# Optimization experiments

Measured on AMD Instinct MI355X. Metric: run time of the kernel, lower is better.

## Reference

```python
import jax, jax.numpy as jnp
import numpy as np

N_IDX = 3_276_800   # total indices shared across all bags
N_BAGS = 16_384     # number of bags (offsets length)
NUM_EMB = 2_000_000 # vocabulary rows per table
DIM = 3             # embedding dim fixed by the module


def setup_inputs() -> dict:
    key = jax.random.key(0)
    k1, k2, k3, k4, k5 = jax.random.split(key, 5)
    eb_input = jax.random.randint(k1, (N_IDX,), 0, NUM_EMB, dtype=jnp.int32)
    eb_offset = jnp.sort(jax.random.randint(k2, (N_BAGS,), 0, N_IDX, dtype=jnp.int32))
    eb_offset = eb_offset.at[0].set(0)  # EmbeddingBag requires offsets[0] == 0
    W0 = jax.random.normal(k3, (NUM_EMB, DIM), dtype=jnp.float32)
    W1 = jax.random.normal(k4, (NUM_EMB, DIM), dtype=jnp.float32)
    W2 = jax.random.normal(k5, (NUM_EMB, DIM), dtype=jnp.float32)
    return {"eb_input": eb_input, "eb_offset": eb_offset, "W0": W0, "W1": W1, "W2": W2}


def _embedding_bag_sum(W, idx, seg_ids, num_bags):
    # gather rows then segment-sum within each bag -> [num_bags, DIM]
    return jax.ops.segment_sum(W[idx], seg_ids, num_segments=num_bags)


def reference(eb_input, eb_offset, W0, W1, W2):
    num_bags = eb_offset.shape[0]
    # bag id of each index position, from the offsets (shared by all 21 bags)
    seg_ids = jnp.searchsorted(eb_offset, jnp.arange(eb_input.shape[0], dtype=eb_offset.dtype), side="right") - 1
    rows = []
    # each group reuses ONE table k times ([module]*k aliases the same module),
    # so cat(k copies of [B,3]).sum(0) == k * per_bag.sum(0)
    for W, mult in ((W0, 5.0), (W1, 10.0), (W2, 6.0)):
        per_bag = _embedding_bag_sum(W, eb_input, seg_ids, num_bags)  # [B, 3]
        rows.append(mult * per_bag.sum(axis=0))                      # [3]
    return jnp.stack(rows)  # [3, 3]
```

## Files before the change

kernel.cpp:

```cpp
#include <hip/hip_runtime.h>


constexpr int BLOCK = 256;
constexpr int WAVES = BLOCK / 64;

constexpr int CBITS = 14;
constexpr int CROWS = 1 << CBITS;
constexpr int MAXKC = 128;
constexpr int GP    = 512;
constexpr int CAPC  = 112;
constexpr int HB    = 1024;
constexpr int SUMG  = 1920;


__global__ __launch_bounds__(BLOCK) void partition_kernel(
    const int* __restrict__ idx,
    unsigned short* __restrict__ region,
    int* __restrict__ counts_T,
    int n, int K)
{
    __shared__ __align__(16) unsigned short buf[MAXKC][CAPC];
    __shared__ int rcnt[MAXKC];

    for (int b = threadIdx.x; b < K; b += BLOCK) rcnt[b] = 0;
    __syncthreads();

    const int g = blockIdx.x;
    const int4* idx4 = (const int4*)idx;
    const int n4 = n >> 2;
    const int per = (n4 + GP - 1) / GP;
    const int start = g * per;
    const int end = min(start + per, n4);

    int4 v[8];
    int cnt = 0;
    for (int i = start + threadIdx.x; i < end; i += BLOCK)
        v[cnt++] = idx4[i];

    for (int j = 0; j < cnt; ++j) {
        int4 w = v[j];
        int xs[4] = {w.x, w.y, w.z, w.w};
#pragma unroll
        for (int h = 0; h < 4; ++h) {
            int b = xs[h] >> CBITS, lo = xs[h] & (CROWS - 1);
            int pos = atomicAdd(&rcnt[b], 1);
            if (pos < CAPC) buf[b][pos] = (unsigned short)lo;
        }
    }
    if (g == 0 && threadIdx.x == 0) {
        for (int i = n4 << 2; i < n; ++i) {
            int x = idx[i];
            int b = x >> CBITS, lo = x & (CROWS - 1);
            int pos = atomicAdd(&rcnt[b], 1);
            if (pos < CAPC) buf[b][pos] = (unsigned short)lo;
        }
    }
    __syncthreads();

    for (int b = threadIdx.x; b < K; b += BLOCK) {
        int c = rcnt[b]; if (c > CAPC) c = CAPC;
        unsigned short* cell = region + ((size_t)b * GP + g) * CAPC;
        const int ng = (c + 7) >> 3;
        for (int j = 0; j < ng; ++j)
            *(uint4*)(cell + j * 8) = *(const uint4*)&buf[b][j * 8];
        counts_T[b * GP + g] = c;
    }
}


__global__ __launch_bounds__(HB) void hist_build_kernel(
    const unsigned short* __restrict__ region,
    const int* __restrict__ counts_T,
    int* __restrict__ counts)
{
    __shared__ unsigned int histp[CROWS / 2];
    __shared__ int scnt[GP];
    const int b = blockIdx.x;

    for (int j = threadIdx.x; j < CROWS / 2; j += HB) histp[j] = 0u;
    for (int g = threadIdx.x; g < GP; g += HB) scnt[g] = counts_T[b * GP + g];
    __syncthreads();

    constexpr int GPC = CAPC / 8;
    constexpr int NG  = GP * GPC;
    const uint4* reg4 = (const uint4*)(region + (size_t)b * GP * CAPC);
    for (int j = threadIdx.x; j < NG; j += HB) {
        int g = j / GPC;
        int q = j - g * GPC;
        uint4 v = reg4[j];
        int valid = scnt[g] - q * 8;
        if (valid >= 8) {
            atomicAdd(&histp[(v.x & 0xFFFFu) >> 1], 1u << (((v.x) & 1u) << 4));
            atomicAdd(&histp[(v.x >> 16) >> 1],     1u << (((v.x >> 16) & 1u) << 4));
            atomicAdd(&histp[(v.y & 0xFFFFu) >> 1], 1u << (((v.y) & 1u) << 4));
            atomicAdd(&histp[(v.y >> 16) >> 1],     1u << (((v.y >> 16) & 1u) << 4));
            atomicAdd(&histp[(v.z & 0xFFFFu) >> 1], 1u << (((v.z) & 1u) << 4));
            atomicAdd(&histp[(v.z >> 16) >> 1],     1u << (((v.z >> 16) & 1u) << 4));
            atomicAdd(&histp[(v.w & 0xFFFFu) >> 1], 1u << (((v.w) & 1u) << 4));
            atomicAdd(&histp[(v.w >> 16) >> 1],     1u << (((v.w >> 16) & 1u) << 4));
        } else if (valid > 0) {
            unsigned vv[4] = {v.x, v.y, v.z, v.w};
#pragma unroll
            for (int h = 0; h < 4; ++h) {
                unsigned lo0 = vv[h] & 0xFFFFu, lo1 = vv[h] >> 16;
                if (valid > 2 * h)     atomicAdd(&histp[lo0 >> 1], 1u << ((lo0 & 1u) << 4));
                if (valid > 2 * h + 1) atomicAdd(&histp[lo1 >> 1], 1u << ((lo1 & 1u) << 4));
            }
        }
    }
    __syncthreads();

    int4* out4 = (int4*)(counts + ((size_t)b << CBITS));
    for (int j = threadIdx.x; j < CROWS / 4; j += HB) {
        unsigned u0 = histp[2 * j], u1 = histp[2 * j + 1];
        int4 val;
        val.x = (int)(u0 & 0xFFFFu);
        val.y = (int)(u0 >> 16);
        val.z = (int)(u1 & 0xFFFFu);
        val.w = (int)(u1 >> 16);
        out4[j] = val;
    }
}


__global__ __launch_bounds__(BLOCK) void weighted_sum_v4(
    const int* __restrict__ counts,
    const float* __restrict__ W0,
    const float* __restrict__ W1,
    const float* __restrict__ W2,
    float* __restrict__ partials,
    int nrows)
{
    float s[9];
#pragma unroll
    for (int k = 0; k < 9; ++k) s[k] = 0.0f;
    const int tid = blockIdx.x * BLOCK + threadIdx.x;
    const int stride = gridDim.x * BLOCK;
    const int nt = nrows >> 2;
    const int4*   c4  = (const int4*)counts;
    const float4* W04 = (const float4*)W0;
    const float4* W14 = (const float4*)W1;
    const float4* W24 = (const float4*)W2;
    for (int t = tid; t < nt; t += stride) {
        int4 ci = c4[t];
        float c0 = (float)ci.x, c1 = (float)ci.y, c2 = (float)ci.z, c3 = (float)ci.w;
        {
            float4 A = W04[3*t], B = W04[3*t+1], C = W04[3*t+2];
            s[0] += c0*A.x + c1*A.w + c2*B.z + c3*C.y;
            s[1] += c0*A.y + c1*B.x + c2*B.w + c3*C.z;
            s[2] += c0*A.z + c1*B.y + c2*C.x + c3*C.w;
        }
        {
            float4 A = W14[3*t], B = W14[3*t+1], C = W14[3*t+2];
            s[3] += c0*A.x + c1*A.w + c2*B.z + c3*C.y;
            s[4] += c0*A.y + c1*B.x + c2*B.w + c3*C.z;
            s[5] += c0*A.z + c1*B.y + c2*C.x + c3*C.w;
        }
        {
            float4 A = W24[3*t], B = W24[3*t+1], C = W24[3*t+2];
            s[6] += c0*A.x + c1*A.w + c2*B.z + c3*C.y;
            s[7] += c0*A.y + c1*B.x + c2*B.w + c3*C.z;
            s[8] += c0*A.z + c1*B.y + c2*C.x + c3*C.w;
        }
    }
    if (tid == 0) {
        for (int r = nt << 2; r < nrows; ++r) {
            float c = (float)counts[r];
            int o = r * 3;
            s[0] += c * W0[o]; s[1] += c * W0[o+1]; s[2] += c * W0[o+2];
            s[3] += c * W1[o]; s[4] += c * W1[o+1]; s[5] += c * W1[o+2];
            s[6] += c * W2[o]; s[7] += c * W2[o+1]; s[8] += c * W2[o+2];
        }
    }
#pragma unroll
    for (int k = 0; k < 9; ++k) {
#pragma unroll
        for (int off = 32; off > 0; off >>= 1)
            s[k] += __shfl_down(s[k], off, 64);
    }
    __shared__ float lds[WAVES][9];
    const int lane = threadIdx.x & 63;
    const int wave = threadIdx.x >> 6;
    if (lane == 0) {
#pragma unroll
        for (int k = 0; k < 9; ++k) lds[wave][k] = s[k];
    }
    __syncthreads();
    if (threadIdx.x < 9) {
        float acc = 0.0f;
#pragma unroll
        for (int w = 0; w < WAVES; ++w) acc += lds[w][threadIdx.x];
        partials[blockIdx.x * 9 + threadIdx.x] = acc;
    }
}


__global__ __launch_bounds__(BLOCK) void zero_counts(int* __restrict__ counts, int n) {
    int4* c4 = (int4*)counts;
    const int n4 = n >> 2;
    const int tid = blockIdx.x * BLOCK + threadIdx.x;
    const int stride = gridDim.x * BLOCK;
    int4 z = {0, 0, 0, 0};
    for (int i = tid; i < n4; i += stride) c4[i] = z;
    if (tid == 0)
        for (int i = n4 << 2; i < n; ++i) counts[i] = 0;
}

__global__ __launch_bounds__(BLOCK) void hist_kernel(
    const int* __restrict__ idx, int* __restrict__ counts, int n) {
    const int4* idx4 = (const int4*)idx;
    const int n4 = n >> 2;
    const int tid = blockIdx.x * BLOCK + threadIdx.x;
    const int stride = gridDim.x * BLOCK;
    for (int i = tid; i < n4; i += stride) {
        int4 v = idx4[i];
        atomicAdd(&counts[v.x], 1);
        atomicAdd(&counts[v.y], 1);
        atomicAdd(&counts[v.z], 1);
        atomicAdd(&counts[v.w], 1);
    }
    if (tid == 0)
        for (int i = n4 << 2; i < n; ++i) atomicAdd(&counts[idx[i]], 1);
}


__global__ __launch_bounds__(BLOCK) void eb_final(
    const float* __restrict__ partials, int nblocks, float* __restrict__ out)
{
    float s[9];
#pragma unroll
    for (int k = 0; k < 9; ++k) s[k] = 0.0f;
    for (int i = threadIdx.x; i < nblocks; i += BLOCK) {
#pragma unroll
        for (int k = 0; k < 9; ++k) s[k] += partials[i * 9 + k];
    }
#pragma unroll
    for (int k = 0; k < 9; ++k) {
#pragma unroll
        for (int off = 32; off > 0; off >>= 1)
            s[k] += __shfl_down(s[k], off, 64);
    }
    __shared__ float lds[WAVES][9];
    const int lane = threadIdx.x & 63;
    const int wave = threadIdx.x >> 6;
    if (lane == 0) {
#pragma unroll
        for (int k = 0; k < 9; ++k) lds[wave][k] = s[k];
    }
    __syncthreads();
    if (threadIdx.x == 0) {
        float tot[9];
#pragma unroll
        for (int k = 0; k < 9; ++k) {
            float acc = 0.0f;
#pragma unroll
            for (int w = 0; w < WAVES; ++w) acc += lds[w][k];
            tot[k] = acc;
        }
        const float mult[3] = {5.0f, 10.0f, 6.0f};
#pragma unroll
        for (int r = 0; r < 3; ++r)
#pragma unroll
            for (int c = 0; c < 3; ++c)
                out[r * 3 + c] = mult[r] * tot[r * 3 + c];
    }
}

extern "C" void kernel_launch(void* const* d_in, const int* in_sizes, int n_in,
                              void* d_out, int out_size, void* d_ws, size_t ws_size,
                              hipStream_t stream) {
    const int*   idx = (const int*)d_in[0];
    const float* W0  = (const float*)d_in[2];
    const float* W1  = (const float*)d_in[3];
    const float* W2  = (const float*)d_in[4];
    float* out = (float*)d_out;

    const int n     = in_sizes[0];
    const int nrows = in_sizes[2] / 3;
    const int K     = (nrows + CROWS - 1) >> CBITS;

    const size_t region_bytes  = (size_t)K * GP * CAPC * sizeof(unsigned short);
    const size_t countsT_bytes = (size_t)K * GP * sizeof(int);
    const size_t counts_bytes  = (size_t)K * CROWS * sizeof(int);
    const size_t partS_bytes   = (size_t)SUMG * 9 * sizeof(float);

    const size_t need_part = region_bytes + countsT_bytes + counts_bytes + partS_bytes;
    const size_t need_hist = (size_t)nrows * sizeof(int) + partS_bytes;

    if (K <= MAXKC && ws_size >= need_part) {
        unsigned short* region   = (unsigned short*)d_ws;
        int*   counts_T = (int*)  ((char*)d_ws + region_bytes);
        int*   counts   = (int*)  ((char*)d_ws + region_bytes + countsT_bytes);
        float* partials = (float*)((char*)d_ws + region_bytes + countsT_bytes + counts_bytes);

        partition_kernel<<<GP, BLOCK, 0, stream>>>(idx, region, counts_T, n, K);
        hist_build_kernel<<<K, HB, 0, stream>>>(region, counts_T, counts);
        weighted_sum_v4<<<SUMG, BLOCK, 0, stream>>>(counts, W0, W1, W2, partials, nrows);
        eb_final<<<1, BLOCK, 0, stream>>>(partials, SUMG, out);
    } else if (ws_size >= need_hist) {
        int*   counts   = (int*)d_ws;
        float* partials = (float*)((char*)d_ws + (size_t)nrows * sizeof(int));
        zero_counts<<<512, BLOCK, 0, stream>>>(counts, nrows);
        hist_kernel<<<1280, BLOCK, 0, stream>>>(idx, counts, n);
        weighted_sum_v4<<<SUMG, BLOCK, 0, stream>>>(counts, W0, W1, W2, partials, nrows);
        eb_final<<<1, BLOCK, 0, stream>>>(partials, SUMG, out);
    }
}
```

Before: 150.2 us.

## Fuse partition, histogram, weighted sum and final reduce into one cooperative kernel

Replaces the four-kernel chain with a single cooperative-launch kernel. Grid-wide syncs separate the partition, per-bucket histogram, weighted-sum and final-reduction phases. The bucket width is halved to 8K rows with a per-block capacity of 64, so each 256-thread block can also build a bucket histogram in LDS. This removes inter-kernel launch gaps and the tail of each small kernel. In exchange it adds grid.sync overhead and runs the bandwidth-bound weighted sum on a fixed 512-block grid instead of 1920 blocks, and it falls back to the atomic path if the cooperative launch fails.

```diff
diff --git a/kernel.cpp b/kernel.cpp
--- a/kernel.cpp
+++ b/kernel.cpp
@@ -1,40 +1,53 @@
 #include <hip/hip_runtime.h>
+#include <hip/hip_cooperative_groups.h>
+
+namespace cg = cooperative_groups;
 
 
 constexpr int BLOCK = 256;
 constexpr int WAVES = BLOCK / 64;
-
-constexpr int CBITS = 14;
+constexpr int GRID  = 512;
+
+constexpr int CBITS = 13;
 constexpr int CROWS = 1 << CBITS;
-constexpr int MAXKC = 128;
-constexpr int GP    = 512;
-constexpr int CAPC  = 112;
-constexpr int HB    = 1024;
-constexpr int SUMG  = 1920;
-
-
-__global__ __launch_bounds__(BLOCK) void partition_kernel(
+constexpr int MAXK  = 256;
+constexpr int CAP   = 64;
+constexpr int GPC   = CAP / 8;
+
+__global__ __launch_bounds__(BLOCK) void fused_kernel(
     const int* __restrict__ idx,
+    const float* __restrict__ W0,
+    const float* __restrict__ W1,
+    const float* __restrict__ W2,
     unsigned short* __restrict__ region,
     int* __restrict__ counts_T,
-    int n, int K)
+    int* __restrict__ counts,
+    float* __restrict__ partials,
+    float* __restrict__ out,
+    int n, int nrows, int K)
 {
-    __shared__ __align__(16) unsigned short buf[MAXKC][CAPC];
-    __shared__ int rcnt[MAXKC];
-
-    for (int b = threadIdx.x; b < K; b += BLOCK) rcnt[b] = 0;
+    __shared__ __align__(16) unsigned short buf[MAXK][CAP];
+    __shared__ int rcnt[MAXK];
+    __shared__ unsigned int histp[CROWS / 2];
+    __shared__ int scnt[GRID];
+    __shared__ float lred[WAVES][9];
+
+    cg::grid_group grid = cg::this_grid();
+    const int g   = blockIdx.x;
+    const int tid = threadIdx.x;
+
+    for (int b = tid; b < K; b += BLOCK) rcnt[b] = 0;
     __syncthreads();
 
-    const int g = blockIdx.x;
     const int4* idx4 = (const int4*)idx;
     const int n4 = n >> 2;
-    const int per = (n4 + GP - 1) / GP;
+    const int per = (n4 + GRID - 1) / GRID;
     const int start = g * per;
     const int end = min(start + per, n4);
 
     int4 v[8];
     int cnt = 0;
-    for (int i = start + threadIdx.x; i < end; i += BLOCK)
+    for (int i = start + tid; i < end; i += BLOCK)
         v[cnt++] = idx4[i];
 
     for (int j = 0; j < cnt; ++j) {
@@ -44,84 +57,208 @@
         for (int h = 0; h < 4; ++h) {
             int b = xs[h] >> CBITS, lo = xs[h] & (CROWS - 1);
             int pos = atomicAdd(&rcnt[b], 1);
-            if (pos < CAPC) buf[b][pos] = (unsigned short)lo;
-        }
-    }
-    if (g == 0 && threadIdx.x == 0) {
+            if (pos < CAP) buf[b][pos] = (unsigned short)lo;
+        }
+    }
+    if (g == 0 && tid == 0) {
         for (int i = n4 << 2; i < n; ++i) {
             int x = idx[i];
             int b = x >> CBITS, lo = x & (CROWS - 1);
             int pos = atomicAdd(&rcnt[b], 1);
-            if (pos < CAPC) buf[b][pos] = (unsigned short)lo;
+            if (pos < CAP) buf[b][pos] = (unsigned short)lo;
         }
     }
     __syncthreads();
 
-    for (int b = threadIdx.x; b < K; b += BLOCK) {
-        int c = rcnt[b]; if (c > CAPC) c = CAPC;
-        unsigned short* cell = region + ((size_t)b * GP + g) * CAPC;
+    for (int b = tid; b < K; b += BLOCK) {
+        int c = rcnt[b]; if (c > CAP) c = CAP;
+        unsigned short* cell = region + ((size_t)b * GRID + g) * CAP;
         const int ng = (c + 7) >> 3;
         for (int j = 0; j < ng; ++j)
             *(uint4*)(cell + j * 8) = *(const uint4*)&buf[b][j * 8];
-        counts_T[b * GP + g] = c;
-    }
-}
-
-
-__global__ __launch_bounds__(HB) void hist_build_kernel(
-    const unsigned short* __restrict__ region,
-    const int* __restrict__ counts_T,
-    int* __restrict__ counts)
-{
-    __shared__ unsigned int histp[CROWS / 2];
-    __shared__ int scnt[GP];
-    const int b = blockIdx.x;
-
-    for (int j = threadIdx.x; j < CROWS / 2; j += HB) histp[j] = 0u;
-    for (int g = threadIdx.x; g < GP; g += HB) scnt[g] = counts_T[b * GP + g];
+        counts_T[b * GRID + g] = c;
+    }
+
+    grid.sync();
+
+    if (g < K) {
+        for (int j = tid; j < CROWS / 2; j += BLOCK) histp[j] = 0u;
+        for (int j = tid; j < GRID; j += BLOCK) scnt[j] = counts_T[g * GRID + j];
+        __syncthreads();
+
+        const uint4* reg4 = (const uint4*)(region + (size_t)g * GRID * CAP);
+        constexpr int NG = GRID * GPC;
+        for (int j = tid; j < NG; j += BLOCK) {
+            int cell = j >> 3;
+            int q = j & 7;
+            uint4 w = reg4[j];
+            int valid = scnt[cell] - q * 8;
+            if (valid >= 8) {
+                atomicAdd(&histp[(w.x & 0xFFFFu) >> 1], 1u << (((w.x) & 1u) << 4));
+                atomicAdd(&histp[(w.x >> 16) >> 1],     1u << (((w.x >> 16) & 1u) << 4));
+                atomicAdd(&histp[(w.y & 0xFFFFu) >> 1], 1u << (((w.y) & 1u) << 4));
+                atomicAdd(&histp[(w.y >> 16) >> 1],     1u << (((w.y >> 16) & 1u) << 4));
+                atomicAdd(&histp[(w.z & 0xFFFFu) >> 1], 1u << (((w.z) & 1u) << 4));
+                atomicAdd(&histp[(w.z >> 16) >> 1],     1u << (((w.z >> 16) & 1u) << 4));
+                atomicAdd(&histp[(w.w & 0xFFFFu) >> 1], 1u << (((w.w) & 1u) << 4));
+                atomicAdd(&histp[(w.w >> 16) >> 1],     1u << (((w.w >> 16) & 1u) << 4));
+            } else if (valid > 0) {
+                unsigned vv[4] = {w.x, w.y, w.z, w.w};
+#pragma unroll
+                for (int h = 0; h < 4; ++h) {
+                    unsigned lo0 = vv[h] & 0xFFFFu, lo1 = vv[h] >> 16;
+                    if (valid > 2 * h)     atomicAdd(&histp[lo0 >> 1], 1u << ((lo0 & 1u) << 4));
+                    if (valid > 2 * h + 1) atomicAdd(&histp[lo1 >> 1], 1u << ((lo1 & 1u) << 4));
+                }
+            }
+        }
+        __syncthreads();
+
+        int4* out4 = (int4*)(counts + ((size_t)g << CBITS));
+        for (int j = tid; j < CROWS / 4; j += BLOCK) {
+            unsigned u0 = histp[2 * j], u1 = histp[2 * j + 1];
+            int4 val;
+            val.x = (int)(u0 & 0xFFFFu);
+            val.y = (int)(u0 >> 16);
+            val.z = (int)(u1 & 0xFFFFu);
+            val.w = (int)(u1 >> 16);
+            out4[j] = val;
+        }
+    }
+
+    grid.sync();
+
+    float s[9];
+#pragma unroll
+    for (int k = 0; k < 9; ++k) s[k] = 0.0f;
+
+    {
+        const int gtid = g * BLOCK + tid;
+        const int stride = GRID * BLOCK;
+        const int nt = nrows >> 2;
+        const int4*   c4  = (const int4*)counts;
+        const float4* W04 = (const float4*)W0;
+        const float4* W14 = (const float4*)W1;
+        const float4* W24 = (const float4*)W2;
+        for (int t = gtid; t < nt; t += stride) {
+            int4 ci = c4[t];
+            float c0 = (float)ci.x, c1 = (float)ci.y, c2 = (float)ci.z, c3 = (float)ci.w;
+            {
+                float4 A = W04[3*t], B = W04[3*t+1], C = W04[3*t+2];
+                s[0] += c0*A.x + c1*A.w + c2*B.z + c3*C.y;
+                s[1] += c0*A.y + c1*B.x + c2*B.w + c3*C.z;
+                s[2] += c0*A.z + c1*B.y + c2*C.x + c3*C.w;
+            }
+            {
+                float4 A = W14[3*t], B = W14[3*t+1], C = W14[3*t+2];
+                s[3] += c0*A.x + c1*A.w + c2*B.z + c3*C.y;
+                s[4] += c0*A.y + c1*B.x + c2*B.w + c3*C.z;
+                s[5] += c0*A.z + c1*B.y + c2*C.x + c3*C.w;
+            }
+            {
+                float4 A = W24[3*t], B = W24[3*t+1], C = W24[3*t+2];
+                s[6] += c0*A.x + c1*A.w + c2*B.z + c3*C.y;
+                s[7] += c0*A.y + c1*B.x + c2*B.w + c3*C.z;
+                s[8] += c0*A.z + c1*B.y + c2*C.x + c3*C.w;
+            }
+        }
+        if (gtid == 0) {
+            for (int r = nt << 2; r < nrows; ++r) {
+                float c = (float)counts[r];
+                int o = r * 3;
+                s[0] += c * W0[o]; s[1] += c * W0[o+1]; s[2] += c * W0[o+2];
+                s[3] += c * W1[o]; s[4] += c * W1[o+1]; s[5] += c * W1[o+2];
+                s[6] += c * W2[o]; s[7] += c * W2[o+1]; s[8] += c * W2[o+2];
+            }
+        }
+    }
+
+#pragma unroll
+    for (int k = 0; k < 9; ++k) {
+#pragma unroll
+        for (int off = 32; off > 0; off >>= 1)
+            s[k] += __shfl_down(s[k], off, 64);
+    }
+    const int lane = tid & 63;
+    const int wave = tid >> 6;
+    if (lane == 0) {
+#pragma unroll
+        for (int k = 0; k < 9; ++k) lred[wave][k] = s[k];
+    }
     __syncthreads();
-
-    constexpr int GPC = CAPC / 8;
-    constexpr int NG  = GP * GPC;
-    const uint4* reg4 = (const uint4*)(region + (size_t)b * GP * CAPC);
-    for (int j = threadIdx.x; j < NG; j += HB) {
-        int g = j / GPC;
-        int q = j - g * GPC;
-        uint4 v = reg4[j];
-        int valid = scnt[g] - q * 8;
-        if (valid >= 8) {
-            atomicAdd(&histp[(v.x & 0xFFFFu) >> 1], 1u << (((v.x) & 1u) << 4));
-            atomicAdd(&histp[(v.x >> 16) >> 1],     1u << (((v.x >> 16) & 1u) << 4));
-            atomicAdd(&histp[(v.y & 0xFFFFu) >> 1], 1u << (((v.y) & 1u) << 4));
-            atomicAdd(&histp[(v.y >> 16) >> 1],     1u << (((v.y >> 16) & 1u) << 4));
-            atomicAdd(&histp[(v.z & 0xFFFFu) >> 1], 1u << (((v.z) & 1u) << 4));
-            atomicAdd(&histp[(v.z >> 16) >> 1],     1u << (((v.z >> 16) & 1u) << 4));
-            atomicAdd(&histp[(v.w & 0xFFFFu) >> 1], 1u << (((v.w) & 1u) << 4));
-            atomicAdd(&histp[(v.w >> 16) >> 1],     1u << (((v.w >> 16) & 1u) << 4));
-        } else if (valid > 0) {
-            unsigned vv[4] = {v.x, v.y, v.z, v.w};
-#pragma unroll
-            for (int h = 0; h < 4; ++h) {
-                unsigned lo0 = vv[h] & 0xFFFFu, lo1 = vv[h] >> 16;
-                if (valid > 2 * h)     atomicAdd(&histp[lo0 >> 1], 1u << ((lo0 & 1u) << 4));
-                if (valid > 2 * h + 1) atomicAdd(&histp[lo1 >> 1], 1u << ((lo1 & 1u) << 4));
-            }
-        }
-    }
-    __syncthreads();
-
-    int4* out4 = (int4*)(counts + ((size_t)b << CBITS));
-    for (int j = threadIdx.x; j < CROWS / 4; j += HB) {
-        unsigned u0 = histp[2 * j], u1 = histp[2 * j + 1];
-        int4 val;
-        val.x = (int)(u0 & 0xFFFFu);
-        val.y = (int)(u0 >> 16);
-        val.z = (int)(u1 & 0xFFFFu);
-        val.w = (int)(u1 >> 16);
-        out4[j] = val;
-    }
-}
-
+    if (tid < 9) {
+        float acc = 0.0f;
+#pragma unroll
+        for (int w = 0; w < WAVES; ++w) acc += lred[w][tid];
+        partials[g * 9 + tid] = acc;
+    }
+
+    grid.sync();
+
+    if (g == 0) {
+        float f[9];
+#pragma unroll
+        for (int k = 0; k < 9; ++k) f[k] = 0.0f;
+        for (int i = tid; i < GRID; i += BLOCK) {
+#pragma unroll
+            for (int k = 0; k < 9; ++k) f[k] += partials[i * 9 + k];
+        }
+#pragma unroll
+        for (int k = 0; k < 9; ++k) {
+#pragma unroll
+            for (int off = 32; off > 0; off >>= 1)
+                f[k] += __shfl_down(f[k], off, 64);
+        }
+        __syncthreads();
+        if (lane == 0) {
+#pragma unroll
+            for (int k = 0; k < 9; ++k) lred[wave][k] = f[k];
+        }
+        __syncthreads();
+        if (tid == 0) {
+            const float mult[3] = {5.0f, 10.0f, 6.0f};
+#pragma unroll
+            for (int r = 0; r < 3; ++r) {
+#pragma unroll
+                for (int c = 0; c < 3; ++c) {
+                    float acc = 0.0f;
+#pragma unroll
+                    for (int w = 0; w < WAVES; ++w) acc += lred[w][r * 3 + c];
+                    out[r * 3 + c] = mult[r] * acc;
+                }
+            }
+        }
+    }
+}
+
+
+__global__ __launch_bounds__(BLOCK) void zero_counts(int* __restrict__ counts, int n) {
+    int4* c4 = (int4*)counts;
+    const int n4 = n >> 2;
+    const int tid = blockIdx.x * BLOCK + threadIdx.x;
+    const int stride = gridDim.x * BLOCK;
+    int4 z = {0, 0, 0, 0};
+    for (int i = tid; i < n4; i += stride) c4[i] = z;
+    if (tid == 0)
+        for (int i = n4 << 2; i < n; ++i) counts[i] = 0;
+}
+
+__global__ __launch_bounds__(BLOCK) void hist_kernel(
+    const int* __restrict__ idx, int* __restrict__ counts, int n) {
+    const int4* idx4 = (const int4*)idx;
+    const int n4 = n >> 2;
+    const int tid = blockIdx.x * BLOCK + threadIdx.x;
+    const int stride = gridDim.x * BLOCK;
+    for (int i = tid; i < n4; i += stride) {
+        int4 v = idx4[i];
+        atomicAdd(&counts[v.x], 1);
+        atomicAdd(&counts[v.y], 1);
+        atomicAdd(&counts[v.z], 1);
+        atomicAdd(&counts[v.w], 1);
+    }
+    if (tid == 0)
+        for (int i = n4 << 2; i < n; ++i) atomicAdd(&counts[idx[i]], 1);
+}
 
 __global__ __launch_bounds__(BLOCK) void weighted_sum_v4(
     const int* __restrict__ counts,
@@ -194,36 +331,6 @@
     }
 }
 
-
-__global__ __launch_bounds__(BLOCK) void zero_counts(int* __restrict__ counts, int n) {
-    int4* c4 = (int4*)counts;
-    const int n4 = n >> 2;
-    const int tid = blockIdx.x * BLOCK + threadIdx.x;
-    const int stride = gridDim.x * BLOCK;
-    int4 z = {0, 0, 0, 0};
-    for (int i = tid; i < n4; i += stride) c4[i] = z;
-    if (tid == 0)
-        for (int i = n4 << 2; i < n; ++i) counts[i] = 0;
-}
-
-__global__ __launch_bounds__(BLOCK) void hist_kernel(
-    const int* __restrict__ idx, int* __restrict__ counts, int n) {
-    const int4* idx4 = (const int4*)idx;
-    const int n4 = n >> 2;
-    const int tid = blockIdx.x * BLOCK + threadIdx.x;
-    const int stride = gridDim.x * BLOCK;
-    for (int i = tid; i < n4; i += stride) {
-        int4 v = idx4[i];
-        atomicAdd(&counts[v.x], 1);
-        atomicAdd(&counts[v.y], 1);
-        atomicAdd(&counts[v.z], 1);
-        atomicAdd(&counts[v.w], 1);
-    }
-    if (tid == 0)
-        for (int i = n4 << 2; i < n; ++i) atomicAdd(&counts[idx[i]], 1);
-}
-
-
 __global__ __launch_bounds__(BLOCK) void eb_final(
     const float* __restrict__ partials, int nblocks, float* __restrict__ out)
 {
@@ -275,34 +382,40 @@
     const float* W2  = (const float*)d_in[4];
     float* out = (float*)d_out;
 
-    const int n     = in_sizes[0];
-    const int nrows = in_sizes[2] / 3;
-    const int K     = (nrows + CROWS - 1) >> CBITS;
-
-    const size_t region_bytes  = (size_t)K * GP * CAPC * sizeof(unsigned short);
-    const size_t countsT_bytes = (size_t)K * GP * sizeof(int);
+    int n     = in_sizes[0];
+    int nrows = in_sizes[2] / 3;
+    int K     = (nrows + CROWS - 1) >> CBITS;
+
+    const size_t region_bytes  = (size_t)K * GRID * CAP * sizeof(unsigned short);
+    const size_t countsT_bytes = (size_t)K * GRID * sizeof(int);
     const size_t counts_bytes  = (size_t)K * CROWS * sizeof(int);
-    const size_t partS_bytes   = (size_t)SUMG * 9 * sizeof(float);
-
-    const size_t need_part = region_bytes + countsT_bytes + counts_bytes + partS_bytes;
-    const size_t need_hist = (size_t)nrows * sizeof(int) + partS_bytes;
-
-    if (K <= MAXKC && ws_size >= need_part) {
+    const size_t partG_bytes   = (size_t)GRID * 9 * sizeof(float);
+    const size_t need_coop = region_bytes + countsT_bytes + counts_bytes + partG_bytes;
+    const size_t need_hist = (size_t)nrows * sizeof(int) + (size_t)1920 * 9 * sizeof(float);
+
+    bool launched = false;
+    if (K <= MAXK && ws_size >= need_coop) {
         unsigned short* region   = (unsigned short*)d_ws;
         int*   counts_T = (int*)  ((char*)d_ws + region_bytes);
         int*   counts   = (int*)  ((char*)d_ws + region_bytes + countsT_bytes);
         float* partials = (float*)((char*)d_ws + region_bytes + countsT_bytes + counts_bytes);
 
-        partition_kernel<<<GP, BLOCK, 0, stream>>>(idx, region, counts_T, n, K);
-        hist_build_kernel<<<K, HB, 0, stream>>>(region, counts_T, counts);
-        weighted_sum_v4<<<SUMG, BLOCK, 0, stream>>>(counts, W0, W1, W2, partials, nrows);
-        eb_final<<<1, BLOCK, 0, stream>>>(partials, SUMG, out);
-    } else if (ws_size >= need_hist) {
+        void* args[] = {
+            (void*)&idx, (void*)&W0, (void*)&W1, (void*)&W2,
+            (void*)&region, (void*)&counts_T, (void*)&counts, (void*)&partials,
+            (void*)&out, (void*)&n, (void*)&nrows, (void*)&K
+        };
+        hipError_t err = hipLaunchCooperativeKernel(
+            (const void*)fused_kernel, dim3(GRID), dim3(BLOCK), args, 0, stream);
+        launched = (err == hipSuccess);
+    }
+
+    if (!launched && ws_size >= need_hist) {
         int*   counts   = (int*)d_ws;
         float* partials = (float*)((char*)d_ws + (size_t)nrows * sizeof(int));
         zero_counts<<<512, BLOCK, 0, stream>>>(counts, nrows);
         hist_kernel<<<1280, BLOCK, 0, stream>>>(idx, counts, n);
-        weighted_sum_v4<<<SUMG, BLOCK, 0, stream>>>(counts, W0, W1, W2, partials, nrows);
-        eb_final<<<1, BLOCK, 0, stream>>>(partials, SUMG, out);
-    }
-}
+        weighted_sum_v4<<<1920, BLOCK, 0, stream>>>(counts, W0, W1, W2, partials, nrows);
+        eb_final<<<1, BLOCK, 0, stream>>>(partials, 1920, out);
+    }
+}
```

New measurement: 340.5 us. 127% more time.
